# Kernel tuning notes

Measured on AMD Instinct MI355X. Metric: run time of the kernel, lower is better.

Reference implementation:

```python
import jax, jax.numpy as jnp
import numpy as np

B, NN, F, H = 8, 1024, 256, 8
D = F // H
SCALE = D ** -0.5


def setup_inputs() -> dict:
    key = jax.random.key(0)
    ks = jax.random.split(key, 12)
    s = 0.02
    inp = {
        'ndata': jax.random.normal(ks[0], (B, NN, F), jnp.float32),
        'N': NN,
        'attn_bias': jax.random.normal(ks[1], (B, NN, NN, H), jnp.float32),
        'attn_mask': jax.random.randint(ks[2], (B, NN, NN), 0, 2).astype(bool),
        'Wq': jax.random.normal(ks[3], (F, F), jnp.float32) * s,
        'bq': jnp.zeros((F,), jnp.float32),
        'Wk': jax.random.normal(ks[4], (F, F), jnp.float32) * s,
        'bk': jnp.zeros((F,), jnp.float32),
        'Wv': jax.random.normal(ks[5], (F, F), jnp.float32) * s,
        'bv': jnp.zeros((F,), jnp.float32),
        'Wo': jax.random.normal(ks[6], (F, F), jnp.float32) * s,
        'bo': jnp.zeros((F,), jnp.float32),
    }
    return inp


def reference(ndata, N, attn_bias, attn_mask, Wq, bq, Wk, bk, Wv, bv, Wo, bo):
    b, n, f = ndata.shape
    # QKV projections (torch nn.Linear: x @ W.T + b), split heads
    q = (ndata @ Wq.T + bq).reshape(b, n, H, D) * SCALE
    k = (ndata @ Wk.T + bk).reshape(b, n, H, D)
    v = (ndata @ Wv.T + bv).reshape(b, n, H, D)
    # scores: (b, q, k, h) matching torch layout after its transposes
    scores = jnp.einsum('bqhd,bkhd->bqkh', q, k)
    scores = scores + attn_bias  # additive bias
    # original code force-unmasks column 0 so every row has a valid entry
    mask = attn_mask.at[:, :, 0].set(False)
    scores = jnp.where(mask[..., None], -jnp.inf, scores)
    attn = jax.nn.softmax(scores, axis=2)  # softmax over keys
    out = jnp.einsum('bqkh,bkhd->bqhd', attn, v).reshape(b, n, f)
    return out @ Wo.T + bo
```

## Files before the change

### kernel.cpp

```cpp
#include <hip/hip_runtime.h>
#include <hip/hip_bf16.h>

typedef __attribute__((ext_vector_type(8))) short short8;
typedef __attribute__((ext_vector_type(4))) float f32x4;

#define MFMA16(a,b,c) __builtin_amdgcn_mfma_f32_16x16x32_bf16((a),(b),(c),0,0,0)

static __device__ __forceinline__ unsigned int f2bf(float f){
    unsigned int u = __float_as_uint(f);
    u += 0x7FFFu + ((u >> 16) & 1u);
    return u >> 16;
}

static __device__ __forceinline__ short8 pack8(float4 a, float4 b){
    short8 r;
    r[0]=(short)f2bf(a.x); r[1]=(short)f2bf(a.y);
    r[2]=(short)f2bf(a.z); r[3]=(short)f2bf(a.w);
    r[4]=(short)f2bf(b.x); r[5]=(short)f2bf(b.y);
    r[6]=(short)f2bf(b.z); r[7]=(short)f2bf(b.w);
    return r;
}

__global__ __launch_bounds__(256) void qkv_mask_k(
    const float* __restrict__ nd,
    const float* __restrict__ Wqp, const float* __restrict__ bqp,
    const float* __restrict__ Wkp, const float* __restrict__ bkp,
    const float* __restrict__ Wvp, const float* __restrict__ bvp,
    unsigned short* __restrict__ qout, unsigned short* __restrict__ kout,
    unsigned short* __restrict__ vtout,
    const unsigned int* __restrict__ m, unsigned int* __restrict__ bmout)
{
    __shared__ __align__(16) unsigned short xl[64*264];
    const int tid  = threadIdx.x;

    if (blockIdx.x >= 384){
        __shared__ int any_hi;
        const int lane = tid & 63;
        const unsigned int gbase = (blockIdx.x - 384)*256u + tid;
        if (tid == 0) any_hi = 0;
        unsigned int wv[8]; unsigned int acc = 0;
        #pragma unroll
        for (int it = 0; it < 8; ++it){
            wv[it] = __builtin_nontemporal_load(m + it*262144u + gbase);
            acc |= wv[it];
        }
        __syncthreads();
        if (acc & 0xFFFFFF00u) atomicOr(&any_hi, 1);
        __syncthreads();
        if (any_hi == 0){
            for (int it = 0; it < 32; ++it){
                unsigned int idx = it*262144u + gbase;
                unsigned int v = __builtin_nontemporal_load(m + idx);
                unsigned long long bal = __ballot(v != 0u);
                if (lane == 0)
                    *(unsigned long long*)(bmout + (idx >> 5)) = bal;
            }
        } else {
            #pragma unroll
            for (int it = 0; it < 8; ++it){
                unsigned int idx = it*262144u + gbase;
                unsigned int v = wv[it];
                unsigned int nib = (v | (v>>7) | (v>>14) | (v>>21)) & 0xFu;
                unsigned int x = nib << ((lane & 7)*4);
                x |= (unsigned int)__shfl_xor((int)x, 1);
                x |= (unsigned int)__shfl_xor((int)x, 2);
                x |= (unsigned int)__shfl_xor((int)x, 4);
                if ((lane & 7) == 0)
                    bmout[idx >> 3] = x;
            }
        }
        return;
    }

    const int bi   = blockIdx.x;
    const int kind = bi >> 7;
    const int R0   = (bi & 127) * 64;
    const int b    = R0 >> 10;
    const int n0   = R0 & 1023;

    #pragma unroll
    for (int it = 0; it < 16; ++it){
        int f4 = it*256 + tid;
        int r = f4 >> 6, c4 = f4 & 63;
        float4 v = *(const float4*)(nd + (size_t)(R0+r)*256 + c4*4);
        unsigned int lo = f2bf(v.x) | (f2bf(v.y) << 16);
        unsigned int hi = f2bf(v.z) | (f2bf(v.w) << 16);
        *(uint2*)&xl[r*264 + c4*4] = make_uint2(lo, hi);
    }
    __syncthreads();

    const int lane = tid & 63;
    const int w  = tid >> 6;
    const int ln = lane & 15;
    const int g  = lane >> 4;
    const int ow = w * 64;

    f32x4 acc[4][4];
    #pragma unroll
    for (int a=0;a<4;++a){
        #pragma unroll
        for (int c=0;c<4;++c) acc[a][c] = (f32x4){0.f,0.f,0.f,0.f};
    }

    if (kind < 2){
        const float* W  = kind ? Wkp : Wqp;
        const float* bb = kind ? bkp : bqp;
        unsigned short* op = kind ? kout : qout;
        const float scl = kind ? 1.0f : 0.17677669529663687f;
        for (int kk = 0; kk < 8; ++kk){
            short8 wf[4], xf[4];
            #pragma unroll
            for (int ot=0; ot<4; ++ot){
                const float* wp = W + (size_t)(ow + ot*16 + ln)*256 + kk*32 + g*8;
                wf[ot] = pack8(*(const float4*)wp, *(const float4*)(wp+4));
            }
            #pragma unroll
            for (int nt=0; nt<4; ++nt)
                xf[nt] = *(const short8*)&xl[(nt*16+ln)*264 + kk*32 + g*8];
            #pragma unroll
            for (int ot=0; ot<4; ++ot){
                #pragma unroll
                for (int nt=0; nt<4; ++nt)
                    acc[ot][nt] = MFMA16(wf[ot], xf[nt], acc[ot][nt]);
            }
        }
        #pragma unroll
        for (int ot=0; ot<4; ++ot){
            int o0 = ow + ot*16 + g*4;
            int h = o0 >> 5, d0 = o0 & 31;
            float4 b4 = *(const float4*)(bb + o0);
            #pragma unroll
            for (int nt=0; nt<4; ++nt){
                int n = n0 + nt*16 + ln;
                unsigned int lo = f2bf((acc[ot][nt][0]+b4.x)*scl) | (f2bf((acc[ot][nt][1]+b4.y)*scl)<<16);
                unsigned int hi = f2bf((acc[ot][nt][2]+b4.z)*scl) | (f2bf((acc[ot][nt][3]+b4.w)*scl)<<16);
                *(uint2*)(op + ((size_t)(b*8+h)*1024 + n)*32 + d0) = make_uint2(lo,hi);
            }
        }
    } else {
        for (int kk = 0; kk < 8; ++kk){
            short8 wf[4], xf[4];
            #pragma unroll
            for (int ot=0; ot<4; ++ot){
                const float* wp = Wvp + (size_t)(ow + ot*16 + ln)*256 + kk*32 + g*8;
                wf[ot] = pack8(*(const float4*)wp, *(const float4*)(wp+4));
            }
            #pragma unroll
            for (int nt=0; nt<4; ++nt)
                xf[nt] = *(const short8*)&xl[(nt*16+ln)*264 + kk*32 + g*8];
            #pragma unroll
            for (int nt=0; nt<4; ++nt){
                #pragma unroll
                for (int ot=0; ot<4; ++ot)
                    acc[nt][ot] = MFMA16(xf[nt], wf[ot], acc[nt][ot]);
            }
        }
        #pragma unroll
        for (int nt=0; nt<4; ++nt){
            int nb = n0 + nt*16 + g*4;
            #pragma unroll
            for (int ot=0; ot<4; ++ot){
                int o = ow + ot*16 + ln;
                int h = o >> 5, d = o & 31;
                float bvv = bvp[o];
                unsigned int lo = f2bf(acc[nt][ot][0]+bvv) | (f2bf(acc[nt][ot][1]+bvv)<<16);
                unsigned int hi = f2bf(acc[nt][ot][2]+bvv) | (f2bf(acc[nt][ot][3]+bvv)<<16);
                *(uint2*)(vtout + ((size_t)(b*8+h)*32 + d)*1024 + nb) = make_uint2(lo,hi);
            }
        }
    }
}

__global__ __launch_bounds__(512, 4) void attn_k(
    const unsigned short* __restrict__ qbuf, const unsigned short* __restrict__ kbuf,
    const unsigned short* __restrict__ vtbuf, const float* __restrict__ bias,
    const unsigned int* __restrict__ bm, unsigned short* __restrict__ ab)
{
    __shared__ __align__(16) float bs[8704];
    const int tid  = threadIdx.x;
    const int bi   = blockIdx.x;
    const int b    = bi >> 6;
    const int q0   = (bi & 63) * 16;
    const int lane = tid & 63;
    const int w    = tid >> 6;
    const int ln   = lane & 15;
    const int g    = lane >> 4;

    const short8 qf = *(const short8*)(qbuf + ((size_t)(b*8+w)*1024 + q0 + ln)*32 + g*8);

    const int kperm = ((ln >> 2) << 3) + (ln & 3);
    const unsigned short* kp = kbuf  + ((size_t)(b*8+w)*1024 + kperm)*32 + g*8;
    const unsigned short* vp = vtbuf + ((size_t)(b*8+w)*32   + ln)*1024 + g*8;
    const unsigned int*  bmp = bm + (size_t)(b*1024 + q0 + ln)*32;

    const int sq  = tid >> 5;
    const float* bgp = bias + (size_t)(b*1024 + q0 + sq)*8192 + (tid & 31)*4;
    const int hqb = (tid & 1)*4*1088 + sq*68;
    const int kpw = (tid & 31) >> 1;
    const int rb0 = w*1088 + ln*68 + 8*g;

    f32x4 acc0 = (f32x4){0.f,0.f,0.f,0.f};
    f32x4 acc1 = (f32x4){0.f,0.f,0.f,0.f};
    float lsum = 0.f;
    const f32x4 z4 = {0.f,0.f,0.f,0.f};

    f32x4 br0, br1, br2, br3;
    short8 kn0, kn1, kn2, kn3;
    unsigned int bm0, bm1;

#define LOAD_ALL(cc) do { int c_ = (cc); \
    br0 = __builtin_nontemporal_load((const f32x4*)(bgp + (size_t)c_*512)); \
    br1 = __builtin_nontemporal_load((const f32x4*)(bgp + (size_t)c_*512 + 128)); \
    br2 = __builtin_nontemporal_load((const f32x4*)(bgp + (size_t)c_*512 + 256)); \
    br3 = __builtin_nontemporal_load((const f32x4*)(bgp + (size_t)c_*512 + 384)); \
    kn0 = *(const short8*)(kp + c_*2048); \
    kn1 = *(const short8*)(kp + c_*2048 + 128); \
    kn2 = *(const short8*)(kp + c_*2048 + 1024); \
    kn3 = *(const short8*)(kp + c_*2048 + 1152); \
    bm0 = bmp[2*c_]; bm1 = bmp[2*c_+1]; } while(0)

#define STAGE1(R, IT) do { int kw_ = (IT)*16 + kpw; \
    bs[hqb        + kw_] = R[0]; \
    bs[hqb + 1088 + kw_] = R[1]; \
    bs[hqb + 2176 + kw_] = R[2]; \
    bs[hqb + 3264 + kw_] = R[3]; } while(0)

#define CHUNK_HALF(K0, K1, BMW, KH, VOFF) do { \
    f32x4 s0 = MFMA16(K0, qf, z4);    \
    f32x4 s1 = MFMA16(K1, qf, z4);    \
    f32x4 blo = *(const f32x4*)&bs[rb0 + (KH)*32]; \
    f32x4 bhi = *(const f32x4*)&bs[rb0 + (KH)*32 + 4]; \
    short8 vf0 = *(const short8*)(vp + (VOFF)); \
    short8 vf1 = *(const short8*)(vp + (VOFF) + 16*1024); \
    unsigned int mb_ = (BMW) >> (g*8); \
    float e0 = __expf(s0[0] + blo[0]); e0 = ((mb_>>0)&1u) ? 0.f : e0; \
    float e1 = __expf(s0[1] + blo[1]); e1 = ((mb_>>1)&1u) ? 0.f : e1; \
    float e2 = __expf(s0[2] + blo[2]); e2 = ((mb_>>2)&1u) ? 0.f : e2; \
    float e3 = __expf(s0[3] + blo[3]); e3 = ((mb_>>3)&1u) ? 0.f : e3; \
    float e4 = __expf(s1[0] + bhi[0]); e4 = ((mb_>>4)&1u) ? 0.f : e4; \
    float e5 = __expf(s1[1] + bhi[1]); e5 = ((mb_>>5)&1u) ? 0.f : e5; \
    float e6 = __expf(s1[2] + bhi[2]); e6 = ((mb_>>6)&1u) ? 0.f : e6; \
    float e7 = __expf(s1[3] + bhi[3]); e7 = ((mb_>>7)&1u) ? 0.f : e7; \
    lsum += ((e0+e1)+(e2+e3)) + ((e4+e5)+(e6+e7)); \
    int4 pw_ = make_int4( \
        (int)(f2bf(e0) | (f2bf(e1)<<16)), (int)(f2bf(e2) | (f2bf(e3)<<16)), \
        (int)(f2bf(e4) | (f2bf(e5)<<16)), (int)(f2bf(e6) | (f2bf(e7)<<16))); \
    short8 pf_ = *(short8*)&pw_; \
    acc0 = MFMA16(vf0, pf_, acc0); \
    acc1 = MFMA16(vf1, pf_, acc1); } while(0)

    LOAD_ALL(0);
    bm0 &= ~1u;

    #pragma unroll 1
    for (int cc = 0; cc < 16; ++cc){
        STAGE1(br0, 0); STAGE1(br1, 1); STAGE1(br2, 2); STAGE1(br3, 3);
        short8 ck0 = kn0, ck1 = kn1, ck2 = kn2, ck3 = kn3;
        unsigned int cb0 = bm0, cb1 = bm1;
        if (cc + 1 < 16) LOAD_ALL(cc + 1);
        __syncthreads();

        CHUNK_HALF(ck0, ck1, cb0, 0, cc*64);
        CHUNK_HALF(ck2, ck3, cb1, 1, cc*64 + 32);
        __syncthreads();
    }

    float ps = lsum;
    ps += __shfl_xor(ps, 16);
    ps += __shfl_xor(ps, 32);
    float inv = 1.0f / ps;
    {
        int n = q0 + ln;
        unsigned int lo0 = f2bf(acc0[0]*inv) | (f2bf(acc0[1]*inv)<<16);
        unsigned int hi0 = f2bf(acc0[2]*inv) | (f2bf(acc0[3]*inv)<<16);
        *(uint2*)(ab + ((size_t)(b*1024 + n))*256 + w*32 + g*4) = make_uint2(lo0,hi0);
        unsigned int lo1 = f2bf(acc1[0]*inv) | (f2bf(acc1[1]*inv)<<16);
        unsigned int hi1 = f2bf(acc1[2]*inv) | (f2bf(acc1[3]*inv)<<16);
        *(uint2*)(ab + ((size_t)(b*1024 + n))*256 + w*32 + 16 + g*4) = make_uint2(lo1,hi1);
    }
#undef LOAD_ALL
#undef STAGE1
#undef CHUNK_HALF
}

__global__ __launch_bounds__(256) void oproj_k(
    const unsigned short* __restrict__ ab, const float* __restrict__ Wop,
    const float* __restrict__ bop, float* __restrict__ out)
{
    __shared__ __align__(16) unsigned short al[32*264];
    const int tid = threadIdx.x;
    const int R0 = blockIdx.x * 32;
    #pragma unroll
    for (int it=0; it<4; ++it){
        int f8 = it*256 + tid;
        int r = f8 >> 5, c8 = f8 & 31;
        *(short8*)&al[r*264 + c8*8] = *(const short8*)(ab + (size_t)(R0+r)*256 + c8*8);
    }
    __syncthreads();
    const int lane = tid & 63;
    const int w = tid >> 6, ln = lane & 15, g = lane >> 4;
    const int ow = w*64;
    f32x4 acc[4][2];
    #pragma unroll
    for (int a=0;a<4;++a){ acc[a][0]=(f32x4){0.f,0.f,0.f,0.f}; acc[a][1]=(f32x4){0.f,0.f,0.f,0.f}; }
    for (int kk=0;kk<8;++kk){
        short8 wf[4], xf[2];
        #pragma unroll
        for (int ot=0;ot<4;++ot){
            const float* wp = Wop + (size_t)(ow+ot*16+ln)*256 + kk*32 + g*8;
            wf[ot] = pack8(*(const float4*)wp, *(const float4*)(wp+4));
        }
        #pragma unroll
        for (int nt=0;nt<2;++nt)
            xf[nt] = *(const short8*)&al[(nt*16+ln)*264 + kk*32 + g*8];
        #pragma unroll
        for (int ot=0;ot<4;++ot){
            #pragma unroll
            for (int nt=0;nt<2;++nt)
                acc[ot][nt] = MFMA16(wf[ot], xf[nt], acc[ot][nt]);
        }
    }
    #pragma unroll
    for (int ot=0;ot<4;++ot){
        int o0 = ow + ot*16 + g*4;
        float4 b4 = *(const float4*)(bop + o0);
        #pragma unroll
        for (int nt=0;nt<2;++nt){
            int n = R0 + nt*16 + ln;
            float4 res;
            res.x = acc[ot][nt][0] + b4.x;
            res.y = acc[ot][nt][1] + b4.y;
            res.z = acc[ot][nt][2] + b4.z;
            res.w = acc[ot][nt][3] + b4.w;
            *(float4*)(out + (size_t)n*256 + o0) = res;
        }
    }
}

extern "C" void kernel_launch(void* const* d_in, const int* in_sizes, int n_in,
                              void* d_out, int out_size, void* d_ws, size_t ws_size,
                              hipStream_t stream)
{
    (void)in_sizes; (void)n_in; (void)out_size; (void)ws_size;
    const float* nd   = (const float*)d_in[0];
    const float* bias = (const float*)d_in[2];
    const int* mask   = (const int*)d_in[3];
    const float* Wq = (const float*)d_in[4];
    const float* bq = (const float*)d_in[5];
    const float* Wk = (const float*)d_in[6];
    const float* bk = (const float*)d_in[7];
    const float* Wv = (const float*)d_in[8];
    const float* bv = (const float*)d_in[9];
    const float* Wo = (const float*)d_in[10];
    const float* bo = (const float*)d_in[11];
    float* out = (float*)d_out;

    const size_t ELEMS = (size_t)8*8*1024*32;
    unsigned short* qb  = (unsigned short*)d_ws;
    unsigned short* kb  = qb  + ELEMS;
    unsigned short* vtb = kb  + ELEMS;
    unsigned short* ab  = vtb + ELEMS;
    unsigned int* bmw   = (unsigned int*)(ab + ELEMS);

    qkv_mask_k<<<1408, 256, 0, stream>>>(nd, Wq, bq, Wk, bk, Wv, bv,
                                         qb, kb, vtb,
                                         (const unsigned int*)mask, bmw);
    attn_k<<<512, 512, 0, stream>>>(qb, kb, vtb, bias, bmw, ab);
    oproj_k<<<256, 256, 0, stream>>>(ab, Wo, bo, out);
}
```

Before: 137.3 us.

## Double-buffer bias staging in attention with smaller chunks and non-draining barriers

The attention kernel now processes 32 key chunks of 32 instead of 16 chunks of 64. Bias tiles go into a double-buffered LDS area, and global loads run two chunks ahead, so each iteration needs one barrier instead of two. The barrier is custom inline asm that waits only on LDS counters, so outstanding global bias loads are not drained at each sync. K and mask loads move inside the compute step and are no longer prefetched, which may expose their latency. Register use and per-chunk work both shrink.

```diff
diff --git a/kernel.cpp b/kernel.cpp
--- a/kernel.cpp
+++ b/kernel.cpp
@@ -171,12 +171,15 @@
     }
 }
 
+#define BARRIER_NODRAIN() \
+    asm volatile("s_waitcnt lgkmcnt(0)\n\ts_barrier" ::: "memory")
+
 __global__ __launch_bounds__(512, 4) void attn_k(
     const unsigned short* __restrict__ qbuf, const unsigned short* __restrict__ kbuf,
     const unsigned short* __restrict__ vtbuf, const float* __restrict__ bias,
     const unsigned int* __restrict__ bm, unsigned short* __restrict__ ab)
 {
-    __shared__ __align__(16) float bs[8704];
+    __shared__ __align__(16) float bs[9216];
     const int tid  = threadIdx.x;
     const int bi   = blockIdx.x;
     const int b    = bi >> 6;
@@ -195,44 +198,40 @@
 
     const int sq  = tid >> 5;
     const float* bgp = bias + (size_t)(b*1024 + q0 + sq)*8192 + (tid & 31)*4;
-    const int hqb = (tid & 1)*4*1088 + sq*68;
+    const int hqb = (tid & 1)*4*576 + sq*36;
     const int kpw = (tid & 31) >> 1;
-    const int rb0 = w*1088 + ln*68 + 8*g;
+    const int rb0 = w*576 + ln*36 + 8*g;
 
     f32x4 acc0 = (f32x4){0.f,0.f,0.f,0.f};
     f32x4 acc1 = (f32x4){0.f,0.f,0.f,0.f};
     float lsum = 0.f;
     const f32x4 z4 = {0.f,0.f,0.f,0.f};
 
-    f32x4 br0, br1, br2, br3;
-    short8 kn0, kn1, kn2, kn3;
-    unsigned int bm0, bm1;
-
-#define LOAD_ALL(cc) do { int c_ = (cc); \
-    br0 = __builtin_nontemporal_load((const f32x4*)(bgp + (size_t)c_*512)); \
-    br1 = __builtin_nontemporal_load((const f32x4*)(bgp + (size_t)c_*512 + 128)); \
-    br2 = __builtin_nontemporal_load((const f32x4*)(bgp + (size_t)c_*512 + 256)); \
-    br3 = __builtin_nontemporal_load((const f32x4*)(bgp + (size_t)c_*512 + 384)); \
-    kn0 = *(const short8*)(kp + c_*2048); \
-    kn1 = *(const short8*)(kp + c_*2048 + 128); \
-    kn2 = *(const short8*)(kp + c_*2048 + 1024); \
-    kn3 = *(const short8*)(kp + c_*2048 + 1152); \
-    bm0 = bmp[2*c_]; bm1 = bmp[2*c_+1]; } while(0)
-
-#define STAGE1(R, IT) do { int kw_ = (IT)*16 + kpw; \
-    bs[hqb        + kw_] = R[0]; \
-    bs[hqb + 1088 + kw_] = R[1]; \
-    bs[hqb + 2176 + kw_] = R[2]; \
-    bs[hqb + 3264 + kw_] = R[3]; } while(0)
-
-#define CHUNK_HALF(K0, K1, BMW, KH, VOFF) do { \
-    f32x4 s0 = MFMA16(K0, qf, z4);    \
-    f32x4 s1 = MFMA16(K1, qf, z4);    \
-    f32x4 blo = *(const f32x4*)&bs[rb0 + (KH)*32]; \
-    f32x4 bhi = *(const f32x4*)&bs[rb0 + (KH)*32 + 4]; \
-    short8 vf0 = *(const short8*)(vp + (VOFF)); \
-    short8 vf1 = *(const short8*)(vp + (VOFF) + 16*1024); \
-    unsigned int mb_ = (BMW) >> (g*8); \
+    f32x4 br0, br1;
+
+#define LOADB(cc) do { int c_ = (cc); \
+    br0 = __builtin_nontemporal_load((const f32x4*)(bgp + (size_t)c_*256)); \
+    br1 = __builtin_nontemporal_load((const f32x4*)(bgp + (size_t)c_*256 + 128)); } while(0)
+
+#define STAGE_TO(BUF) do { float* bb_ = bs + (BUF)*4608; \
+    { int kw_ = kpw;      bb_[hqb+kw_]=br0[0]; bb_[hqb+576+kw_]=br0[1]; \
+                          bb_[hqb+1152+kw_]=br0[2]; bb_[hqb+1728+kw_]=br0[3]; } \
+    { int kw_ = 16+kpw;   bb_[hqb+kw_]=br1[0]; bb_[hqb+576+kw_]=br1[1]; \
+                          bb_[hqb+1152+kw_]=br1[2]; bb_[hqb+1728+kw_]=br1[3]; } } while(0)
+
+#define COMPUTE(C, BUF) do { int c_ = (C); \
+    short8 kf0 = *(const short8*)(kp + c_*1024); \
+    short8 kf1 = *(const short8*)(kp + c_*1024 + 128); \
+    unsigned int bmw_ = bmp[c_]; \
+    if (c_ == 0) bmw_ &= ~1u;            \
+    f32x4 s0 = MFMA16(kf0, qf, z4);      \
+    f32x4 s1 = MFMA16(kf1, qf, z4);      \
+    const float* bb_ = bs + (BUF)*4608; \
+    f32x4 blo = *(const f32x4*)&bb_[rb0]; \
+    f32x4 bhi = *(const f32x4*)&bb_[rb0 + 4]; \
+    short8 vf0 = *(const short8*)(vp + c_*32); \
+    short8 vf1 = *(const short8*)(vp + c_*32 + 16*1024); \
+    unsigned int mb_ = bmw_ >> (g*8); \
     float e0 = __expf(s0[0] + blo[0]); e0 = ((mb_>>0)&1u) ? 0.f : e0; \
     float e1 = __expf(s0[1] + blo[1]); e1 = ((mb_>>1)&1u) ? 0.f : e1; \
     float e2 = __expf(s0[2] + blo[2]); e2 = ((mb_>>2)&1u) ? 0.f : e2; \
@@ -249,20 +248,18 @@
     acc0 = MFMA16(vf0, pf_, acc0); \
     acc1 = MFMA16(vf1, pf_, acc1); } while(0)
 
-    LOAD_ALL(0);
-    bm0 &= ~1u;
+    LOADB(0);
+    STAGE_TO(0);
+    LOADB(1);
+    BARRIER_NODRAIN();
 
     #pragma unroll 1
-    for (int cc = 0; cc < 16; ++cc){
-        STAGE1(br0, 0); STAGE1(br1, 1); STAGE1(br2, 2); STAGE1(br3, 3);
-        short8 ck0 = kn0, ck1 = kn1, ck2 = kn2, ck3 = kn3;
-        unsigned int cb0 = bm0, cb1 = bm1;
-        if (cc + 1 < 16) LOAD_ALL(cc + 1);
-        __syncthreads();
-
-        CHUNK_HALF(ck0, ck1, cb0, 0, cc*64);
-        CHUNK_HALF(ck2, ck3, cb1, 1, cc*64 + 32);
-        __syncthreads();
+    for (int c = 0; c < 32; ++c){
+        const int cur = c & 1;
+        if (c + 1 < 32) STAGE_TO(cur ^ 1);
+        if (c + 2 < 32) LOADB(c + 2);
+        COMPUTE(c, cur);
+        BARRIER_NODRAIN();
     }
 
     float ps = lsum;
@@ -278,9 +275,9 @@
         unsigned int hi1 = f2bf(acc1[2]*inv) | (f2bf(acc1[3]*inv)<<16);
         *(uint2*)(ab + ((size_t)(b*1024 + n))*256 + w*32 + 16 + g*4) = make_uint2(lo1,hi1);
     }
-#undef LOAD_ALL
-#undef STAGE1
-#undef CHUNK_HALF
+#undef LOADB
+#undef STAGE_TO
+#undef COMPUTE
 }
 
 __global__ __launch_bounds__(256) void oproj_k(
```

Result: slower. 141.8 us (+3.3%).
